# Kernel optimization log

Measured on AMD Instinct MI355X. Metric: run time of the kernel, lower is better.

## Reference

```python
import jax, jax.numpy as jnp
import numpy as np

B, T, V, D = 128, 128, 64, 32
Q, E, PLM = 5, 8, 768
D_STATIC, N_CLASS = 16, 2
ALPHA = 0.5


def _glorot(key, shape):
    lim = (6.0 / (shape[-2] + shape[-1])) ** 0.5
    return jax.random.uniform(key, shape, jnp.float32, -lim, lim)


def setup_inputs() -> dict:
    key = jax.random.key(0)
    ks = jax.random.split(key, 30)
    data = jax.random.normal(ks[0], (B, T, V), jnp.float32)
    mask = (jax.random.uniform(ks[1], (B, T, V)) < 0.3).astype(jnp.float32)
    P = jnp.concatenate([data, mask], axis=-1)  # [b, t, 2v]
    return {
        "P": P,
        "P_static": jax.random.normal(ks[2], (B, D_STATIC), jnp.float32),
        "P_avg_interval": jax.random.uniform(ks[3], (B, T, V)) * 10.0,
        "P_length": jax.random.randint(ks[4], (B, 1), T // 2, T + 1),
        "P_time": jax.random.uniform(ks[5], (B, T)),
        "P_var_plm_rep_tensor": jax.random.normal(ks[6], (V, PLM), jnp.float32),
        # Value_Encoder: Linear(1, D) + ReLU
        "w_val": _glorot(ks[7], (1, D))[0], "b_val": jnp.zeros((D,), jnp.float32),
        # Time_Encoder: periodic Linear(1, D-1), linear Linear(1, 1)
        "w_per": _glorot(ks[8], (1, D - 1))[0], "b_per": jnp.zeros((D - 1,), jnp.float32),
        "w_lin": _glorot(ks[9], (1, 1))[0], "b_lin": jnp.zeros((1,), jnp.float32),
        "emb1": jax.random.normal(ks[10], (V, D), jnp.float32),
        # prior_to_state MLP: PLM -> 2D -> Q
        "Ws1": _glorot(ks[11], (PLM, 2 * D)), "bs1": jnp.zeros((2 * D,), jnp.float32),
        "Ws2": _glorot(ks[12], (2 * D, Q)), "bs2": jnp.zeros((Q,), jnp.float32),
        # prior_to_graph MLP: PLM -> 2D -> E
        "Wg1": _glorot(ks[13], (PLM, 2 * D)), "bg1": jnp.zeros((2 * D,), jnp.float32),
        "Wg2": _glorot(ks[14], (2 * D, E)), "bg2": jnp.zeros((E,), jnp.float32),
        "rarity_W": jax.random.normal(ks[15], (V, V), jnp.float32),
        # hypernet gate params (nodes_num == Q): W [Q, 2D+1, D], b [Q, D]
        "Wu": _glorot(ks[16], (Q, 2 * D + 1, D)), "bu": _glorot(ks[17], (Q, D)),
        "Wr": _glorot(ks[18], (Q, 2 * D + 1, D)), "br": _glorot(ks[19], (Q, D)),
        "Wcand": _glorot(ks[20], (Q, 2 * D + 1, D)), "bcand": _glorot(ks[21], (Q, D)),
        # static embedding + classifier
        "W_se": _glorot(ks[22], (D_STATIC, V)), "b_se": jnp.zeros((V,), jnp.float32),
        "Wc1": _glorot(ks[23], (2 * V, 200)), "bc1": jnp.zeros((200,), jnp.float32),
        "Wc2": _glorot(ks[24], (200, N_CLASS)), "bc2": jnp.zeros((N_CLASS,), jnp.float32),
    }


def _forward(P, P_static, P_avg_interval, P_length, P_time, P_var_plm_rep_tensor,
             w_val, b_val, w_per, b_per, w_lin, b_lin, emb1,
             Ws1, bs1, Ws2, bs2, Wg1, bg1, Wg2, bg2, rarity_W,
             Wu, bu, Wr, br, Wcand, bcand, W_se, b_se, Wc1, bc1, Wc2, bc2):
    b, t, v2 = P.shape
    v = v2 // 2
    d = emb1.shape[1]
    data, mask = P[:, :, :v], P[:, :, v:]            # [b,t,v] each
    mk = mask[..., None]
    # embeddings: value + absolute time + node embedding, all masked
    value_emb = jax.nn.relu(data[..., None] * w_val + b_val) * mk          # [b,t,v,d]
    tt = P_time[:, :, None, None]                                          # [b,t,1,1]
    time_emb = jnp.concatenate([tt * w_lin + b_lin,
                                jnp.sin(tt * w_per + b_per)], -1) * mk     # [b,t,v,d]
    obs_emb = (value_emb + time_emb + emb1[None, None]) * mk               # [b,t,v,d]

    # PLM-prior hypernet vectors (identical across batch -> computed once, broadcast)
    var_vector = jax.nn.relu(P_var_plm_rep_tensor @ Ws1 + bs1) @ Ws2 + bs2  # [v,Q]
    gvec = jax.nn.relu(P_var_plm_rep_tensor @ Wg1 + bg1) @ Wg2 + bg2        # [v,E]
    gvec = gvec / jnp.maximum(jnp.linalg.norm(gvec, axis=-1, keepdims=True), 1e-12)
    adj = jax.nn.softmax(gvec @ gvec.T, axis=-1)                            # [v,v]

    var_total_obs = mask.sum(axis=1)                                        # [b,v]
    eye = jnp.eye(v, dtype=P.dtype)
    lengths = P_length[:, 0].astype(jnp.int32)                              # [b]

    def gate(inp, W, bb):
        # hypernet-generated per-node GRU gate: einsum('nd,dio->nio') + bmm, fused
        return (jnp.einsum('bvi,vq,qio->bvo', inp, var_vector, W)
                + jnp.einsum('vq,qo->vo', var_vector, bb))

    def step(carry, xs):
        h, out = carry
        cur_obs, m, cur_avg, s = xs
        rarity = ALPHA * jnp.tanh(cur_avg / (var_total_obs + 1.0))          # [b,v]
        rsm = -rarity_W * jnp.abs(rarity[:, :, None] - rarity[:, None, :])  # [b,v,v]
        amask = m[:, :, None] * m[:, None, :]   # rows of unobserved zeroed, observed cols = 1
        cur_adj = adj * (1.0 + rsm) * amask * (1.0 - eye) + eye             # [b,v,v]
        x = jnp.concatenate([cur_obs, rarity[..., None]], -1)               # [b,v,d+1]
        comb = jnp.einsum('bij,bjk->bik', cur_adj, jnp.concatenate([x, h], -1))
        r = jax.nn.sigmoid(gate(comb, Wr, br))
        u = jax.nn.sigmoid(gate(comb, Wu, bu))
        h_r = r * h  # original mutates h[nodes_ind] = r*h[nodes_ind] before candidate
        cand = jnp.tanh(gate(jnp.concatenate([x, h_r], -1), Wcand, bcand))
        h_new = (1.0 - u) * h_r + u * cand
        h = jnp.where((m > 0.5)[..., None], h_new, h)  # scatter only observed nodes
        out = jnp.where((s == lengths - 1)[:, None, None], h, out)
        return (h, out), None

    xs = (jnp.moveaxis(obs_emb, 1, 0), jnp.moveaxis(mask, 1, 0),
          jnp.moveaxis(P_avg_interval, 1, 0), jnp.arange(t, dtype=jnp.int32))
    h0 = jnp.zeros((b, v, d), P.dtype)
    (_, output), _ = jax.lax.scan(step, (h0, jnp.zeros_like(h0)), xs)

    static_emb = P_static @ W_se + b_se                                     # [b,v]
    feat = jnp.concatenate([output.sum(-1), static_emb], -1)                # [b,2v]
    return jax.nn.relu(feat @ Wc1 + bc1) @ Wc2 + bc2                        # [b,n_class]


def reference(P, P_static, P_avg_interval, P_length, P_time, P_var_plm_rep_tensor,
              w_val, b_val, w_per, b_per, w_lin, b_lin, emb1,
              Ws1, bs1, Ws2, bs2, Wg1, bg1, Wg2, bg2, rarity_W,
              Wu, bu, Wr, br, Wcand, bcand, W_se, b_se, Wc1, bc1, Wc2, bc2):
    return _forward(P, P_static, P_avg_interval, P_length, P_time, P_var_plm_rep_tensor,
                    w_val, b_val, w_per, b_per, w_lin, b_lin, emb1,
                    Ws1, bs1, Ws2, bs2, Wg1, bg1, Wg2, bg2, rarity_W,
                    Wu, bu, Wr, br, Wcand, bcand, W_se, b_se, Wc1, bc1, Wc2, bc2)
```

## Files before the change

kernel.cpp:

```cpp
#include <hip/hip_runtime.h>
#include <hip/hip_bf16.h>
#include <math.h>

#define BB 128
#define TT 128
#define VV 64
#define DD 32
#define NQ 5

typedef short bf16x8 __attribute__((ext_vector_type(8)));
typedef float f32x4 __attribute__((ext_vector_type(4)));

#define MFMA(a,b,c) __builtin_amdgcn_mfma_f32_16x16x32_bf16(a,b,c,0,0,0)

__device__ __forceinline__ float sigm(float x){ return 1.0f/(1.0f+__expf(-x)); }
__device__ __forceinline__ float tanhfast(float x){ return 2.0f/(1.0f+__expf(-2.0f*x)) - 1.0f; }
__device__ __forceinline__ unsigned short f2bf(float x){
  unsigned u = __float_as_uint(x);
  u += 0x7FFFu + ((u>>16)&1u);
  return (unsigned short)(u>>16);
}
__device__ __forceinline__ float bf2f(unsigned short h){
  return __uint_as_float(((unsigned)h)<<16);
}

union bfu { bf16x8 v; unsigned u[4]; unsigned short s[8]; };

__device__ __forceinline__ void split8(const float* x, bfu& H, bfu& L){
  #pragma unroll
  for (int i = 0; i < 4; ++i){
    const float a = x[2*i], c = x[2*i+1];
    const __hip_bfloat162 hp = __float22bfloat162_rn(make_float2(a, c));
    unsigned hu; __builtin_memcpy(&hu, &hp, 4);
    H.u[i] = hu;
    const float ah = __uint_as_float(hu << 16);
    const float ch = __uint_as_float(hu & 0xFFFF0000u);
    const __hip_bfloat162 lp = __float22bfloat162_rn(make_float2(a - ah, c - ch));
    unsigned lu; __builtin_memcpy(&lu, &lp, 4);
    L.u[i] = lu;
  }
}

__device__ __forceinline__ void split4(const float* x, unsigned* H, unsigned* L){
  #pragma unroll
  for (int i = 0; i < 2; ++i){
    const float a = x[2*i], c = x[2*i+1];
    const __hip_bfloat162 hp = __float22bfloat162_rn(make_float2(a, c));
    unsigned hu; __builtin_memcpy(&hu, &hp, 4);
    H[i] = hu;
    const float ah = __uint_as_float(hu << 16);
    const float ch = __uint_as_float(hu & 0xFFFF0000u);
    const __hip_bfloat162 lp = __float22bfloat162_rn(make_float2(a - ah, c - ch));
    unsigned lu; __builtin_memcpy(&lu, &lp, 4);
    L[i] = lu;
  }
}


__global__ __launch_bounds__(64)
void k_mlp(const float* __restrict__ Pplm,
           const float* __restrict__ Ws1, const float* __restrict__ bs1,
           const float* __restrict__ Ws2, const float* __restrict__ bs2,
           const float* __restrict__ Wg1, const float* __restrict__ bg1,
           const float* __restrict__ Wg2, const float* __restrict__ bg2,
           float* __restrict__ vv_ws, float* __restrict__ gn_ws)
{
  __shared__ float sH[64], sG[64], sgv[8];
  const int v = blockIdx.x, j = threadIdx.x;
  float a = bs1[j], g = bg1[j];
  for (int k = 0; k < 768; ++k){
    const float p = Pplm[v*768 + k];
    a = fmaf(p, Ws1[k*64 + j], a);
    g = fmaf(p, Wg1[k*64 + j], g);
  }
  sH[j] = fmaxf(a, 0.f);
  sG[j] = fmaxf(g, 0.f);
  __syncthreads();
  if (j < 5){
    float acc = bs2[j];
    for (int k = 0; k < 64; ++k) acc = fmaf(sH[k], Ws2[k*5 + j], acc);
    vv_ws[v*5 + j] = acc;
  }
  if (j < 8){
    float acc = bg2[j];
    for (int k = 0; k < 64; ++k) acc = fmaf(sG[k], Wg2[k*8 + j], acc);
    sgv[j] = acc;
  }
  __syncthreads();
  if (j == 0){
    float n = 0.f;
    for (int e = 0; e < 8; ++e) n += sgv[e]*sgv[e];
    n = fmaxf(sqrtf(n), 1e-12f);
    for (int e = 0; e < 8; ++e) gn_ws[v*8 + e] = sgv[e]/n;
  }
}

__global__ __launch_bounds__(64)
void k_adj(const float* __restrict__ gn_ws, float* __restrict__ adj_ws)
{
  const int v = blockIdx.x, j = threadIdx.x;
  float sc = 0.f;
  #pragma unroll
  for (int e = 0; e < 8; ++e) sc += gn_ws[v*8+e]*gn_ws[j*8+e];
  float mx = sc;
  for (int off = 32; off > 0; off >>= 1) mx = fmaxf(mx, __shfl_xor(mx, off));
  const float ex = __expf(sc - mx);
  float sm = ex;
  for (int off = 32; off > 0; off >>= 1) sm += __shfl_xor(sm, off);
  adj_ws[v*64 + j] = ex / sm;
}

__global__ __launch_bounds__(256)
void k_vto(const float* __restrict__ P, float* __restrict__ vto_ws)
{
  const int idx = blockIdx.x*256 + threadIdx.x;
  if (idx >= BB*VV) return;
  const int b = idx/VV, v = idx%VV;
  float s = 0.f;
  for (int t = 0; t < TT; ++t) s += P[((size_t)(b*TT+t))*128 + 64 + v];
  vto_ws[idx] = s;
}

__global__ __launch_bounds__(256)
void k_bpack(const float* __restrict__ Wr, const float* __restrict__ br,
             const float* __restrict__ Wu, const float* __restrict__ bu,
             const float* __restrict__ Wc, const float* __restrict__ bc,
             unsigned short* __restrict__ Bru, unsigned short* __restrict__ Bcn,
             float* __restrict__ sideRU, float* __restrict__ sideC)
{
  const int idx = blockIdx.x*256 + threadIdx.x;
  if (idx < 20480){
    const int f = idx >> 9, rem = idx & 511, l = rem >> 3, j = rem & 7;
    const int p = f & 1, kt = (f>>1)&1, e = f>>2;
    const int kp = kt*32 + (l>>4)*8 + j;
    const int k = (kp < 32) ? kp : kp + 1;
    const int o = p*16 + (l&15);
    const int q = (e < 5) ? e : e - 5;
    const float* W = (e < 5) ? Wr : Wu;
    Bru[idx] = f2bf(W[(q*65 + k)*32 + o]);
  } else if (idx < 30720){
    const int i2 = idx - 20480;
    const int f = i2 >> 9, rem = i2 & 511, l = rem >> 3, j = rem & 7;
    const int p = f & 1, kt = (f>>1)&1, e = f>>2;
    const int kp = kt*32 + (l>>4)*8 + j;
    const int k = (kp < 32) ? kp : kp + 1;
    const int o = p*16 + (l&15);
    Bcn[i2] = f2bf(Wc[(e*65 + k)*32 + o]);
  } else if (idx < 31360){
    const int i3 = idx - 30720;
    const int e = i3 >> 6, rem = i3 & 63, o = rem >> 1, s = rem & 1;
    const int q = (e < 5) ? e : e - 5;
    float v;
    if (s == 0) v = (e < 5) ? Wr[(q*65 + 32)*32 + o] : Wu[(q*65 + 32)*32 + o];
    else        v = (e < 5) ? br[q*32 + o] : bu[q*32 + o];
    sideRU[i3] = v;
  } else if (idx < 31680){
    const int i4 = idx - 31360;
    const int e = i4 >> 6, rem = i4 & 63, o = rem >> 1, s = rem & 1;
    sideC[i4] = s ? bc[e*32 + o] : Wc[(e*65 + 32)*32 + o];
  }
}


__global__ __launch_bounds__(512, 1)
void tedgn_main(const float* __restrict__ P, const float* __restrict__ Pstatic,
                const float* __restrict__ Pavg, const int* __restrict__ Plen,
                const float* __restrict__ Ptime,
                const float* __restrict__ w_val, const float* __restrict__ b_val,
                const float* __restrict__ w_per, const float* __restrict__ b_per,
                const float* __restrict__ w_lin, const float* __restrict__ b_lin,
                const float* __restrict__ emb1, const float* __restrict__ rarW,
                const float* __restrict__ Wse, const float* __restrict__ bse,
                const float* __restrict__ Wc1, const float* __restrict__ bc1,
                const float* __restrict__ Wc2, const float* __restrict__ bc2,
                const float* __restrict__ vv_ws, const float* __restrict__ adjb_ws,
                const float* __restrict__ vto_ws,
                const unsigned short* __restrict__ Bru_ws,
                const unsigned short* __restrict__ Bc_ws,
                const float* __restrict__ sideRU_ws, const float* __restrict__ sideC_ws,
                float* __restrict__ out)
{
  __shared__ __align__(16) unsigned short B0T[2][2][64][72];
  __shared__ __align__(16) unsigned short s_Wru[20480];
  __shared__ __align__(16) unsigned short s_Wc[10240];
  __shared__ __align__(16) float A1f[4][16][68];
  __shared__ __align__(16) float hrF[4][16][36];
  __shared__ __align__(16) float s_rar[2][64];
  __shared__ __align__(16) float s_m[2][64];
  __shared__ float s_sru[640], s_scd[320];
  __shared__ float s_outf[64][33];
  __shared__ float s_feat[128], s_hid[200];

  const int tid  = threadIdx.x;
  const int lane = tid & 63;
  const int wid  = tid >> 6;
  const int mq   = wid >> 1;
  const int ph   = wid & 1;
  const int l15  = lane & 15;
  const int l16g = lane >> 4;
  const int kgo  = l16g * 8;
  const int R    = mq * 16;
  const int v_own = R + l15;
  const int oo   = ph*16 + l15;
  const int b    = blockIdx.x;
  const int len  = Plen[b];

  for (int i = tid; i < 640; i += 512) s_sru[i] = sideRU_ws[i];
  for (int i = tid; i < 320; i += 512) s_scd[i] = sideC_ws[i];
  {
    const uint4* src1 = (const uint4*)Bru_ws;
    uint4* dst1 = (uint4*)s_Wru;
    for (int i = tid; i < 2560; i += 512) dst1[i] = src1[i];
    const uint4* src2 = (const uint4*)Bc_ws;
    uint4* dst2 = (uint4*)s_Wc;
    for (int i = tid; i < 1280; i += 512) dst2[i] = src2[i];
  }

  float adjb_r[2][8], rarW_r[2][8];
  #pragma unroll
  for (int kt = 0; kt < 2; ++kt)
    #pragma unroll
    for (int j = 0; j < 8; ++j){
      adjb_r[kt][j] = adjb_ws[v_own*64 + kt*32 + kgo + j];
      rarW_r[kt][j] = rarW   [v_own*64 + kt*32 + kgo + j];
    }
  float embr[8], wvr[8], bvr[8], wpr[8], bpr[8];
  #pragma unroll
  for (int j = 0; j < 8; ++j){
    const int d = kgo + j;
    embr[j] = emb1[v_own*DD + d];
    wvr[j]  = w_val[d];
    bvr[j]  = b_val[d];
    wpr[j]  = (d == 0) ? w_lin[0] : w_per[d-1];
    bpr[j]  = (d == 0) ? b_lin[0] : b_per[d-1];
  }
  float vvr[4][NQ];
  #pragma unroll
  for (int j = 0; j < 4; ++j)
    #pragma unroll
    for (int q = 0; q < NQ; ++q)
      vvr[j][q] = vv_ws[(R + l16g*4 + j)*NQ + q];
  const float vto_own = vto_ws[b*VV + v_own];

  float h[4]    = {0.f,0.f,0.f,0.f};
  float outr[4] = {0.f,0.f,0.f,0.f};
  bfu xfH, xfL;
  float rar_own, m_own;

  {
    const float pd = P[(size_t)(b*TT)*128 + v_own];
    const float pm = P[(size_t)(b*TT)*128 + 64 + v_own];
    const float pa = Pavg[(size_t)(b*TT)*VV + v_own];
    const float pt = Ptime[b*TT];
    const float rar_n = 0.5f * tanhfast(pa / (vto_own + 1.f));
    float xv[8];
    #pragma unroll
    for (int j = 0; j < 8; ++j){
      const int d = kgo + j;
      const float tearg = fmaf(pt, wpr[j], bpr[j]);
      const float te = (d == 0) ? tearg : __sinf(tearg);
      const float ve = fmaxf(fmaf(pd, wvr[j], bvr[j]), 0.f);
      xv[j] = (ve + te + embr[j]) * pm;
    }
    split8(xv, xfH, xfL);
    if (ph == 0){
      #pragma unroll
      for (int j = 0; j < 8; ++j){
        B0T[0][0][kgo + j][v_own] = xfH.s[j];
        B0T[0][1][kgo + j][v_own] = xfL.s[j];
      }
      *(uint2*)&B0T[0][0][32 + l15][R + l16g*4] = make_uint2(0u, 0u);
      *(uint2*)&B0T[0][1][32 + l15][R + l16g*4] = make_uint2(0u, 0u);
      if (l16g == 0){
        s_rar[0][v_own] = rar_n;
        s_m[0][v_own]   = pm;
      }
    } else {
      *(uint2*)&B0T[0][0][48 + l15][R + l16g*4] = make_uint2(0u, 0u);
      *(uint2*)&B0T[0][1][48 + l15][R + l16g*4] = make_uint2(0u, 0u);
    }
    rar_own = rar_n;
    m_own   = pm;
  }
  __syncthreads();

  #pragma clang loop unroll(disable)
  for (int t = 0; t < TT; ++t){
    const int cur = t & 1, nxt = cur ^ 1;

    float pd = 0.f, pm = 0.f, pa = 0.f, pt = 0.f;
    const bool more = (t + 1 < TT);
    if (more){
      pd = P[(size_t)(b*TT + t + 1)*128 + v_own];
      pm = P[(size_t)(b*TT + t + 1)*128 + 64 + v_own];
      pa = Pavg[(size_t)(b*TT + t + 1)*VV + v_own];
      pt = Ptime[b*TT + t + 1];
    }

    {
      bfu aAh[2], aAl[2];
      float crar = 0.f;
      #pragma unroll
      for (int kt = 0; kt < 2; ++kt){
        const float4 r0 = *(const float4*)&s_rar[cur][kt*32 + kgo];
        const float4 r1 = *(const float4*)&s_rar[cur][kt*32 + kgo + 4];
        const float4 m0 = *(const float4*)&s_m[cur][kt*32 + kgo];
        const float4 m1 = *(const float4*)&s_m[cur][kt*32 + kgo + 4];
        const float rj[8] = {r0.x,r0.y,r0.z,r0.w,r1.x,r1.y,r1.z,r1.w};
        const float mj[8] = {m0.x,m0.y,m0.z,m0.w,m1.x,m1.y,m1.z,m1.w};
        float av[8];
        #pragma unroll
        for (int j = 0; j < 8; ++j){
          const int k = kt*32 + kgo + j;
          const float e1 = fmaf(-rarW_r[kt][j], fabsf(rar_own - rj[j]), 1.0f);
          const float a  = adjb_r[kt][j] * e1 * (m_own * mj[j]);
          av[j] = (k == v_own) ? 1.0f : a;
          crar = fmaf(av[j], rj[j], crar);
        }
        split8(av, aAh[kt], aAl[kt]);
      }
      crar += __shfl_xor(crar, 16);
      crar += __shfl_xor(crar, 32);
      if (ph == 0 && l16g == 0) A1f[mq][l15][64] = crar;

      #pragma unroll
      for (int ni = 0; ni < 2; ++ni){
        const int n = 2*ph + ni;
        f32x4 acc = {0.f,0.f,0.f,0.f};
        #pragma unroll
        for (int kt = 0; kt < 2; ++kt){
          const bf16x8 bh = *(const bf16x8*)&B0T[cur][0][n*16 + l15][kt*32 + kgo];
          const bf16x8 bl = *(const bf16x8*)&B0T[cur][1][n*16 + l15][kt*32 + kgo];
          acc = MFMA(aAh[kt].v, bh, acc);
          acc = MFMA(aAl[kt].v, bh, acc);
          acc = MFMA(aAh[kt].v, bl, acc);
        }
        const int col = n*16 + l15;
        #pragma unroll
        for (int j = 0; j < 4; ++j) A1f[mq][l16g*4 + j][col] = acc[j];
      }
    }
    __syncthreads();

    float hr[4], uu[4];
    {
      bfu aH[2], aL[2];
      #pragma unroll
      for (int kt = 0; kt < 2; ++kt){
        float xv[8];
        *(float4*)&xv[0] = *(const float4*)&A1f[mq][l15][kt*32 + kgo];
        *(float4*)&xv[4] = *(const float4*)&A1f[mq][l15][kt*32 + kgo + 4];
        split8(xv, aH[kt], aL[kt]);
      }
      float a64f[4];
      #pragma unroll
      for (int j = 0; j < 4; ++j) a64f[j] = A1f[mq][l16g*4 + j][64];

      f32x4 ag[10];
      #pragma unroll
      for (int e = 0; e < 10; ++e){
        const float2 wb = *(const float2*)&s_sru[e*64 + oo*2];
        #pragma unroll
        for (int j = 0; j < 4; ++j) ag[e][j] = fmaf(a64f[j], wb.x, wb.y);
      }
      #pragma unroll
      for (int e = 0; e < 10; ++e){
        const bf16x8 w0 = *(const bf16x8*)&s_Wru[(((e*2+0)*2+ph)*64 + lane)*8];
        const bf16x8 w1 = *(const bf16x8*)&s_Wru[(((e*2+1)*2+ph)*64 + lane)*8];
        ag[e] = MFMA(aH[0].v, w0, ag[e]);
        ag[e] = MFMA(aL[0].v, w0, ag[e]);
        ag[e] = MFMA(aH[1].v, w1, ag[e]);
        ag[e] = MFMA(aL[1].v, w1, ag[e]);
      }
      #pragma unroll
      for (int j = 0; j < 4; ++j){
        const float pr = vvr[j][0]*ag[0][j] + vvr[j][1]*ag[1][j]
                       + vvr[j][2]*ag[2][j] + vvr[j][3]*ag[3][j]
                       + vvr[j][4]*ag[4][j];
        hr[j] = sigm(pr) * h[j];
        hrF[mq][l16g*4 + j][oo] = hr[j];
      }
      #pragma unroll
      for (int j = 0; j < 4; ++j){
        const float pu = vvr[j][0]*ag[5][j] + vvr[j][1]*ag[6][j]
                       + vvr[j][2]*ag[7][j] + vvr[j][3]*ag[8][j]
                       + vvr[j][4]*ag[9][j];
        uu[j] = sigm(pu);
      }
    }
    __syncthreads();

    {
      bfu hH, hL;
      {
        float hv[8];
        *(float4*)&hv[0] = *(const float4*)&hrF[mq][l15][kgo];
        *(float4*)&hv[4] = *(const float4*)&hrF[mq][l15][kgo + 4];
        split8(hv, hH, hL);
      }
      float rar_cj[4], m_cj[4];
      #pragma unroll
      for (int j = 0; j < 4; ++j){
        rar_cj[j] = s_rar[cur][R + l16g*4 + j];
        m_cj[j]   = s_m[cur][R + l16g*4 + j];
      }
      f32x4 ag[5];
      #pragma unroll
      for (int e = 0; e < 5; ++e){
        const float2 wb = *(const float2*)&s_scd[e*64 + oo*2];
        #pragma unroll
        for (int j = 0; j < 4; ++j) ag[e][j] = fmaf(rar_cj[j], wb.x, wb.y);
      }
      #pragma unroll
      for (int e = 0; e < 5; ++e){
        const bf16x8 w0 = *(const bf16x8*)&s_Wc[(((e*2+0)*2+ph)*64 + lane)*8];
        const bf16x8 w1 = *(const bf16x8*)&s_Wc[(((e*2+1)*2+ph)*64 + lane)*8];
        ag[e] = MFMA(xfH.v, w0, ag[e]);
        ag[e] = MFMA(xfL.v, w0, ag[e]);
        ag[e] = MFMA(hH.v,  w1, ag[e]);
        ag[e] = MFMA(hL.v,  w1, ag[e]);
      }
      const bool snap = (t == len - 1);
      #pragma unroll
      for (int j = 0; j < 4; ++j){
        const float pc = vvr[j][0]*ag[0][j] + vvr[j][1]*ag[1][j]
                       + vvr[j][2]*ag[2][j] + vvr[j][3]*ag[3][j]
                       + vvr[j][4]*ag[4][j];
        const float cd = tanhfast(pc);
        const float hn = fmaf(uu[j], cd - hr[j], hr[j]);
        const float hf = (m_cj[j] > 0.5f) ? hn : h[j];
        h[j] = hf;
        if (snap) outr[j] = hf;
      }
      {
        unsigned H2[2], L2[2];
        split4(h, H2, L2);
        *(uint2*)&B0T[nxt][0][32 + oo][R + l16g*4] = make_uint2(H2[0], H2[1]);
        *(uint2*)&B0T[nxt][1][32 + oo][R + l16g*4] = make_uint2(L2[0], L2[1]);
      }
      if (more){
        const float rar_n = 0.5f * tanhfast(pa / (vto_own + 1.f));
        float xv[8];
        #pragma unroll
        for (int j = 0; j < 8; ++j){
          const int d = kgo + j;
          const float tearg = fmaf(pt, wpr[j], bpr[j]);
          const float te = (d == 0) ? tearg : __sinf(tearg);
          const float ve = fmaxf(fmaf(pd, wvr[j], bvr[j]), 0.f);
          xv[j] = (ve + te + embr[j]) * pm;
        }
        split8(xv, xfH, xfL);
        if (ph == 0){
          #pragma unroll
          for (int j = 0; j < 8; ++j){
            B0T[nxt][0][kgo + j][v_own] = xfH.s[j];
            B0T[nxt][1][kgo + j][v_own] = xfL.s[j];
          }
          if (l16g == 0){
            s_rar[nxt][v_own] = rar_n;
            s_m[nxt][v_own]   = pm;
          }
        }
        rar_own = rar_n;
        m_own   = pm;
      }
    }
    __syncthreads();
  }

  #pragma unroll
  for (int j = 0; j < 4; ++j)
    s_outf[R + l16g*4 + j][oo] = outr[j];
  __syncthreads();
  if (tid < VV){
    float s = 0.f;
    #pragma unroll
    for (int d = 0; d < DD; ++d) s += s_outf[tid][d];
    s_feat[tid] = s;
  } else if (tid < 2*VV){
    const int v = tid - VV;
    float se = bse[v];
    #pragma unroll
    for (int k = 0; k < 16; ++k) se = fmaf(Pstatic[b*16 + k], Wse[k*VV + v], se);
    s_feat[VV + v] = se;
  }
  __syncthreads();
  if (tid < 200){
    float a = bc1[tid];
    for (int k = 0; k < 128; ++k) a = fmaf(s_feat[k], Wc1[k*200 + tid], a);
    s_hid[tid] = fmaxf(a, 0.f);
  }
  __syncthreads();
  if (tid < 2){
    float a = bc2[tid];
    for (int k = 0; k < 200; ++k) a = fmaf(s_hid[k], Wc2[k*2 + tid], a);
    out[b*2 + tid] = a;
  }
}


extern "C" void kernel_launch(void* const* d_in, const int* in_sizes, int n_in,
                              void* d_out, int out_size, void* d_ws, size_t ws_size,
                              hipStream_t stream) {
  (void)in_sizes; (void)n_in; (void)out_size; (void)ws_size;
  const float* P       = (const float*)d_in[0];
  const float* Pstatic = (const float*)d_in[1];
  const float* Pavg    = (const float*)d_in[2];
  const int*   Plen    = (const int*)  d_in[3];
  const float* Ptime   = (const float*)d_in[4];
  const float* Pplm    = (const float*)d_in[5];
  const float* w_val   = (const float*)d_in[6];
  const float* b_val   = (const float*)d_in[7];
  const float* w_per   = (const float*)d_in[8];
  const float* b_per   = (const float*)d_in[9];
  const float* w_lin   = (const float*)d_in[10];
  const float* b_lin   = (const float*)d_in[11];
  const float* emb1    = (const float*)d_in[12];
  const float* Ws1     = (const float*)d_in[13];
  const float* bs1     = (const float*)d_in[14];
  const float* Ws2     = (const float*)d_in[15];
  const float* bs2     = (const float*)d_in[16];
  const float* Wg1     = (const float*)d_in[17];
  const float* bg1     = (const float*)d_in[18];
  const float* Wg2     = (const float*)d_in[19];
  const float* bg2     = (const float*)d_in[20];
  const float* rarW    = (const float*)d_in[21];
  const float* Wu      = (const float*)d_in[22];
  const float* bu      = (const float*)d_in[23];
  const float* Wr      = (const float*)d_in[24];
  const float* br      = (const float*)d_in[25];
  const float* Wcand   = (const float*)d_in[26];
  const float* bcand   = (const float*)d_in[27];
  const float* Wse     = (const float*)d_in[28];
  const float* bse     = (const float*)d_in[29];
  const float* Wc1     = (const float*)d_in[30];
  const float* bc1     = (const float*)d_in[31];
  const float* Wc2     = (const float*)d_in[32];
  const float* bc2     = (const float*)d_in[33];

  float* ws = (float*)d_ws;
  float*          vv_ws   = ws;
  float*          gn_ws   = ws + 320;
  float*          adjb_ws = ws + 832;
  float*          vto_ws  = ws + 4928;
  unsigned short* Bru_ws  = (unsigned short*)(ws + 13120);
  unsigned short* Bc_ws   = (unsigned short*)(ws + 23360);
  float*          sideRU_ws = ws + 28480;
  float*          sideC_ws  = ws + 29120;

  k_mlp  <<<64, 64, 0, stream>>>(Pplm, Ws1, bs1, Ws2, bs2, Wg1, bg1, Wg2, bg2, vv_ws, gn_ws);
  k_adj  <<<64, 64, 0, stream>>>(gn_ws, adjb_ws);
  k_vto  <<<(BB*VV + 255)/256, 256, 0, stream>>>(P, vto_ws);
  k_bpack<<<124, 256, 0, stream>>>(Wr, br, Wu, bu, Wcand, bcand, Bru_ws, Bc_ws, sideRU_ws, sideC_ws);

  tedgn_main<<<BB, 512, 0, stream>>>(P, Pstatic, Pavg, Plen, Ptime,
                                     w_val, b_val, w_per, b_per, w_lin, b_lin,
                                     emb1, rarW, Wse, bse, Wc1, bc1, Wc2, bc2,
                                     vv_ws, adjb_ws, vto_ws,
                                     Bru_ws, Bc_ws, sideRU_ws, sideC_ws,
                                     (float*)d_out);
}
```

Before: 586.2 us.

## Add producer wavefronts to precompute next-step adjacency fragments during recurrence

Grows the block from 8 to 12 wavefronts. The four new producer waves compute the next timestep's adjacency matrix, its bf16 hi/lo split fragments, the rarity-weighted row sums and the input embeddings, and write them into double-buffered shared memory. The worker waves now read these precomputed A fragments instead of rebuilding the adjacency every step, which removes that work from the serial recurrence's critical path. In exchange the block uses more shared memory and threads, producers must keep pace within the existing barrier phases, and the classifier scratch buffers are aliased onto the fragment buffer.

New measurement: 741.5 us. +26.5%, slower.

```diff
diff --git a/kernel.cpp b/kernel.cpp
--- a/kernel.cpp
+++ b/kernel.cpp
@@ -38,21 +38,6 @@
     const __hip_bfloat162 lp = __float22bfloat162_rn(make_float2(a - ah, c - ch));
     unsigned lu; __builtin_memcpy(&lu, &lp, 4);
     L.u[i] = lu;
-  }
-}
-
-__device__ __forceinline__ void split4(const float* x, unsigned* H, unsigned* L){
-  #pragma unroll
-  for (int i = 0; i < 2; ++i){
-    const float a = x[2*i], c = x[2*i+1];
-    const __hip_bfloat162 hp = __float22bfloat162_rn(make_float2(a, c));
-    unsigned hu; __builtin_memcpy(&hu, &hp, 4);
-    H[i] = hu;
-    const float ah = __uint_as_float(hu << 16);
-    const float ch = __uint_as_float(hu & 0xFFFF0000u);
-    const __hip_bfloat162 lp = __float22bfloat162_rn(make_float2(a - ah, c - ch));
-    unsigned lu; __builtin_memcpy(&lu, &lp, 4);
-    L[i] = lu;
   }
 }
 
@@ -162,7 +147,7 @@
 }
 
 
-__global__ __launch_bounds__(512, 1)
+__global__ __launch_bounds__(768, 1)
 void tedgn_main(const float* __restrict__ P, const float* __restrict__ Pstatic,
                 const float* __restrict__ Pavg, const int* __restrict__ Plen,
                 const float* __restrict__ Ptime,
@@ -183,18 +168,19 @@
   __shared__ __align__(16) unsigned short B0T[2][2][64][72];
   __shared__ __align__(16) unsigned short s_Wru[20480];
   __shared__ __align__(16) unsigned short s_Wc[10240];
+  __shared__ __align__(16) unsigned short sFragA[2][4][2][2][64][8];
   __shared__ __align__(16) float A1f[4][16][68];
   __shared__ __align__(16) float hrF[4][16][36];
   __shared__ __align__(16) float s_rar[2][64];
   __shared__ __align__(16) float s_m[2][64];
+  __shared__ float s_crar[2][64];
   __shared__ float s_sru[640], s_scd[320];
-  __shared__ float s_outf[64][33];
-  __shared__ float s_feat[128], s_hid[200];
 
   const int tid  = threadIdx.x;
   const int lane = tid & 63;
   const int wid  = tid >> 6;
-  const int mq   = wid >> 1;
+  const bool isWork = (wid < 8);
+  const int mq   = isWork ? (wid >> 1) : (wid - 8);
   const int ph   = wid & 1;
   const int l15  = lane & 15;
   const int l16g = lane >> 4;
@@ -205,25 +191,17 @@
   const int b    = blockIdx.x;
   const int len  = Plen[b];
 
-  for (int i = tid; i < 640; i += 512) s_sru[i] = sideRU_ws[i];
-  for (int i = tid; i < 320; i += 512) s_scd[i] = sideC_ws[i];
+  for (int i = tid; i < 640; i += 768) s_sru[i] = sideRU_ws[i];
+  for (int i = tid; i < 320; i += 768) s_scd[i] = sideC_ws[i];
   {
     const uint4* src1 = (const uint4*)Bru_ws;
     uint4* dst1 = (uint4*)s_Wru;
-    for (int i = tid; i < 2560; i += 512) dst1[i] = src1[i];
+    for (int i = tid; i < 2560; i += 768) dst1[i] = src1[i];
     const uint4* src2 = (const uint4*)Bc_ws;
     uint4* dst2 = (uint4*)s_Wc;
-    for (int i = tid; i < 1280; i += 512) dst2[i] = src2[i];
-  }
-
-  float adjb_r[2][8], rarW_r[2][8];
-  #pragma unroll
-  for (int kt = 0; kt < 2; ++kt)
-    #pragma unroll
-    for (int j = 0; j < 8; ++j){
-      adjb_r[kt][j] = adjb_ws[v_own*64 + kt*32 + kgo + j];
-      rarW_r[kt][j] = rarW   [v_own*64 + kt*32 + kgo + j];
-    }
+    for (int i = tid; i < 1280; i += 768) dst2[i] = src2[i];
+  }
+
   float embr[8], wvr[8], bvr[8], wpr[8], bpr[8];
   #pragma unroll
   for (int j = 0; j < 8; ++j){
@@ -234,25 +212,36 @@
     wpr[j]  = (d == 0) ? w_lin[0] : w_per[d-1];
     bpr[j]  = (d == 0) ? b_lin[0] : b_per[d-1];
   }
+
+  float adjb_r[2][8], rarW_r[2][8];
+  float vto_own = 0.f;
   float vvr[4][NQ];
-  #pragma unroll
-  for (int j = 0; j < 4; ++j)
-    #pragma unroll
-    for (int q = 0; q < NQ; ++q)
-      vvr[j][q] = vv_ws[(R + l16g*4 + j)*NQ + q];
-  const float vto_own = vto_ws[b*VV + v_own];
+  if (!isWork){
+    #pragma unroll
+    for (int kt = 0; kt < 2; ++kt)
+      #pragma unroll
+      for (int j = 0; j < 8; ++j){
+        adjb_r[kt][j] = adjb_ws[v_own*64 + kt*32 + kgo + j];
+        rarW_r[kt][j] = rarW   [v_own*64 + kt*32 + kgo + j];
+      }
+    vto_own = vto_ws[b*VV + v_own];
+  } else {
+    #pragma unroll
+    for (int j = 0; j < 4; ++j)
+      #pragma unroll
+      for (int q = 0; q < NQ; ++q)
+        vvr[j][q] = vv_ws[(R + l16g*4 + j)*NQ + q];
+  }
 
   float h[4]    = {0.f,0.f,0.f,0.f};
   float outr[4] = {0.f,0.f,0.f,0.f};
-  bfu xfH, xfL;
-  float rar_own, m_own;
-
-  {
+  bfu xfH, xfL, xfnH, xfnL;
+  float pp_pd = 0.f, pp_pm = 0.f, pp_pt = 0.f, pp_rar = 0.f;
+
+  if (isWork){
     const float pd = P[(size_t)(b*TT)*128 + v_own];
     const float pm = P[(size_t)(b*TT)*128 + 64 + v_own];
-    const float pa = Pavg[(size_t)(b*TT)*VV + v_own];
     const float pt = Ptime[b*TT];
-    const float rar_n = 0.5f * tanhfast(pa / (vto_own + 1.f));
     float xv[8];
     #pragma unroll
     for (int j = 0; j < 8; ++j){
@@ -264,86 +253,136 @@
     }
     split8(xv, xfH, xfL);
     if (ph == 0){
-      #pragma unroll
-      for (int j = 0; j < 8; ++j){
-        B0T[0][0][kgo + j][v_own] = xfH.s[j];
-        B0T[0][1][kgo + j][v_own] = xfL.s[j];
-      }
       *(uint2*)&B0T[0][0][32 + l15][R + l16g*4] = make_uint2(0u, 0u);
       *(uint2*)&B0T[0][1][32 + l15][R + l16g*4] = make_uint2(0u, 0u);
-      if (l16g == 0){
-        s_rar[0][v_own] = rar_n;
-        s_m[0][v_own]   = pm;
-      }
     } else {
       *(uint2*)&B0T[0][0][48 + l15][R + l16g*4] = make_uint2(0u, 0u);
       *(uint2*)&B0T[0][1][48 + l15][R + l16g*4] = make_uint2(0u, 0u);
     }
-    rar_own = rar_n;
-    m_own   = pm;
+  } else {
+    pp_pd = P[(size_t)(b*TT)*128 + v_own];
+    pp_pm = P[(size_t)(b*TT)*128 + 64 + v_own];
+    const float pa = Pavg[(size_t)(b*TT)*VV + v_own];
+    pp_pt = Ptime[b*TT];
+    pp_rar = 0.5f * tanhfast(pa / (vto_own + 1.f));
+    if (l16g == 0){
+      s_rar[0][v_own] = pp_rar;
+      s_m[0][v_own]   = pp_pm;
+    }
+  }
+  __syncthreads();
+  if (!isWork){
+    float xv[8];
+    #pragma unroll
+    for (int j = 0; j < 8; ++j){
+      const int d = kgo + j;
+      const float tearg = fmaf(pp_pt, wpr[j], bpr[j]);
+      const float te = (d == 0) ? tearg : __sinf(tearg);
+      const float ve = fmaxf(fmaf(pp_pd, wvr[j], bvr[j]), 0.f);
+      xv[j] = (ve + te + embr[j]) * pp_pm;
+    }
+    bfu xh, xl;
+    split8(xv, xh, xl);
+    #pragma unroll
+    for (int j = 0; j < 8; ++j){
+      B0T[0][0][kgo + j][v_own] = xh.s[j];
+      B0T[0][1][kgo + j][v_own] = xl.s[j];
+    }
+    bfu aAh[2], aAl[2];
+    float crar = 0.f;
+    #pragma unroll
+    for (int kt = 0; kt < 2; ++kt){
+      const float4 r0 = *(const float4*)&s_rar[0][kt*32 + kgo];
+      const float4 r1 = *(const float4*)&s_rar[0][kt*32 + kgo + 4];
+      const float4 m0 = *(const float4*)&s_m[0][kt*32 + kgo];
+      const float4 m1 = *(const float4*)&s_m[0][kt*32 + kgo + 4];
+      const float rj[8] = {r0.x,r0.y,r0.z,r0.w,r1.x,r1.y,r1.z,r1.w};
+      const float mj[8] = {m0.x,m0.y,m0.z,m0.w,m1.x,m1.y,m1.z,m1.w};
+      float av[8];
+      #pragma unroll
+      for (int j = 0; j < 8; ++j){
+        const int k = kt*32 + kgo + j;
+        const float e1 = fmaf(-rarW_r[kt][j], fabsf(pp_rar - rj[j]), 1.0f);
+        const float a  = adjb_r[kt][j] * e1 * (pp_pm * mj[j]);
+        av[j] = (k == v_own) ? 1.0f : a;
+        crar = fmaf(av[j], rj[j], crar);
+      }
+      split8(av, aAh[kt], aAl[kt]);
+    }
+    crar += __shfl_xor(crar, 16);
+    crar += __shfl_xor(crar, 32);
+    if (l16g == 0) s_crar[0][v_own] = crar;
+    #pragma unroll
+    for (int kt = 0; kt < 2; ++kt){
+      *(bf16x8*)&sFragA[0][mq][kt][0][lane][0] = aAh[kt].v;
+      *(bf16x8*)&sFragA[0][mq][kt][1][lane][0] = aAl[kt].v;
+    }
   }
   __syncthreads();
 
   #pragma clang loop unroll(disable)
   for (int t = 0; t < TT; ++t){
     const int cur = t & 1, nxt = cur ^ 1;
-
-    float pd = 0.f, pm = 0.f, pa = 0.f, pt = 0.f;
     const bool more = (t + 1 < TT);
-    if (more){
-      pd = P[(size_t)(b*TT + t + 1)*128 + v_own];
-      pm = P[(size_t)(b*TT + t + 1)*128 + 64 + v_own];
-      pa = Pavg[(size_t)(b*TT + t + 1)*VV + v_own];
-      pt = Ptime[b*TT + t + 1];
-    }
-
-    {
-      bfu aAh[2], aAl[2];
-      float crar = 0.f;
-      #pragma unroll
-      for (int kt = 0; kt < 2; ++kt){
-        const float4 r0 = *(const float4*)&s_rar[cur][kt*32 + kgo];
-        const float4 r1 = *(const float4*)&s_rar[cur][kt*32 + kgo + 4];
-        const float4 m0 = *(const float4*)&s_m[cur][kt*32 + kgo];
-        const float4 m1 = *(const float4*)&s_m[cur][kt*32 + kgo + 4];
-        const float rj[8] = {r0.x,r0.y,r0.z,r0.w,r1.x,r1.y,r1.z,r1.w};
-        const float mj[8] = {m0.x,m0.y,m0.z,m0.w,m1.x,m1.y,m1.z,m1.w};
-        float av[8];
-        #pragma unroll
-        for (int j = 0; j < 8; ++j){
-          const int k = kt*32 + kgo + j;
-          const float e1 = fmaf(-rarW_r[kt][j], fabsf(rar_own - rj[j]), 1.0f);
-          const float a  = adjb_r[kt][j] * e1 * (m_own * mj[j]);
-          av[j] = (k == v_own) ? 1.0f : a;
-          crar = fmaf(av[j], rj[j], crar);
-        }
-        split8(av, aAh[kt], aAl[kt]);
-      }
-      crar += __shfl_xor(crar, 16);
-      crar += __shfl_xor(crar, 32);
-      if (ph == 0 && l16g == 0) A1f[mq][l15][64] = crar;
-
+
+    if (isWork){
+      float pd = 0.f, pm = 0.f, pt = 0.f;
+      if (more){
+        pd = P[(size_t)(b*TT + t + 1)*128 + v_own];
+        pm = P[(size_t)(b*TT + t + 1)*128 + 64 + v_own];
+        pt = Ptime[b*TT + t + 1];
+      }
+      bf16x8 aAh0 = *(const bf16x8*)&sFragA[cur][mq][0][0][lane][0];
+      bf16x8 aAl0 = *(const bf16x8*)&sFragA[cur][mq][0][1][lane][0];
+      bf16x8 aAh1 = *(const bf16x8*)&sFragA[cur][mq][1][0][lane][0];
+      bf16x8 aAl1 = *(const bf16x8*)&sFragA[cur][mq][1][1][lane][0];
       #pragma unroll
       for (int ni = 0; ni < 2; ++ni){
         const int n = 2*ph + ni;
         f32x4 acc = {0.f,0.f,0.f,0.f};
-        #pragma unroll
-        for (int kt = 0; kt < 2; ++kt){
-          const bf16x8 bh = *(const bf16x8*)&B0T[cur][0][n*16 + l15][kt*32 + kgo];
-          const bf16x8 bl = *(const bf16x8*)&B0T[cur][1][n*16 + l15][kt*32 + kgo];
-          acc = MFMA(aAh[kt].v, bh, acc);
-          acc = MFMA(aAl[kt].v, bh, acc);
-          acc = MFMA(aAh[kt].v, bl, acc);
+        {
+          const bf16x8 bh0 = *(const bf16x8*)&B0T[cur][0][n*16 + l15][kgo];
+          const bf16x8 bl0 = *(const bf16x8*)&B0T[cur][1][n*16 + l15][kgo];
+          acc = MFMA(aAh0, bh0, acc);
+          acc = MFMA(aAl0, bh0, acc);
+          acc = MFMA(aAh0, bl0, acc);
+          const bf16x8 bh1 = *(const bf16x8*)&B0T[cur][0][n*16 + l15][32 + kgo];
+          const bf16x8 bl1 = *(const bf16x8*)&B0T[cur][1][n*16 + l15][32 + kgo];
+          acc = MFMA(aAh1, bh1, acc);
+          acc = MFMA(aAl1, bh1, acc);
+          acc = MFMA(aAh1, bl1, acc);
         }
         const int col = n*16 + l15;
         #pragma unroll
         for (int j = 0; j < 4; ++j) A1f[mq][l16g*4 + j][col] = acc[j];
       }
+      if (more){
+        float xv[8];
+        #pragma unroll
+        for (int j = 0; j < 8; ++j){
+          const int d = kgo + j;
+          const float tearg = fmaf(pt, wpr[j], bpr[j]);
+          const float te = (d == 0) ? tearg : __sinf(tearg);
+          const float ve = fmaxf(fmaf(pd, wvr[j], bvr[j]), 0.f);
+          xv[j] = (ve + te + embr[j]) * pm;
+        }
+        split8(xv, xfnH, xfnL);
+      }
+    } else if (more){
+      pp_pd = P[(size_t)(b*TT + t + 1)*128 + v_own];
+      pp_pm = P[(size_t)(b*TT + t + 1)*128 + 64 + v_own];
+      const float pa = Pavg[(size_t)(b*TT + t + 1)*VV + v_own];
+      pp_pt = Ptime[b*TT + t + 1];
+      pp_rar = 0.5f * tanhfast(pa / (vto_own + 1.f));
+      if (l16g == 0){
+        s_rar[nxt][v_own] = pp_rar;
+        s_m[nxt][v_own]   = pp_pm;
+      }
     }
     __syncthreads();
 
     float hr[4], uu[4];
-    {
+    if (isWork){
       bfu aH[2], aL[2];
       #pragma unroll
       for (int kt = 0; kt < 2; ++kt){
@@ -354,7 +393,7 @@
       }
       float a64f[4];
       #pragma unroll
-      for (int j = 0; j < 4; ++j) a64f[j] = A1f[mq][l16g*4 + j][64];
+      for (int j = 0; j < 4; ++j) a64f[j] = s_crar[cur][R + l16g*4 + j];
 
       f32x4 ag[10];
       #pragma unroll
@@ -387,10 +426,56 @@
                        + vvr[j][4]*ag[9][j];
         uu[j] = sigm(pu);
       }
+    } else if (more){
+      float xv[8];
+      #pragma unroll
+      for (int j = 0; j < 8; ++j){
+        const int d = kgo + j;
+        const float tearg = fmaf(pp_pt, wpr[j], bpr[j]);
+        const float te = (d == 0) ? tearg : __sinf(tearg);
+        const float ve = fmaxf(fmaf(pp_pd, wvr[j], bvr[j]), 0.f);
+        xv[j] = (ve + te + embr[j]) * pp_pm;
+      }
+      bfu xh, xl;
+      split8(xv, xh, xl);
+      #pragma unroll
+      for (int j = 0; j < 8; ++j){
+        B0T[nxt][0][kgo + j][v_own] = xh.s[j];
+        B0T[nxt][1][kgo + j][v_own] = xl.s[j];
+      }
+      bfu aAh[2], aAl[2];
+      float crar = 0.f;
+      #pragma unroll
+      for (int kt = 0; kt < 2; ++kt){
+        const float4 r0 = *(const float4*)&s_rar[nxt][kt*32 + kgo];
+        const float4 r1 = *(const float4*)&s_rar[nxt][kt*32 + kgo + 4];
+        const float4 m0 = *(const float4*)&s_m[nxt][kt*32 + kgo];
+        const float4 m1 = *(const float4*)&s_m[nxt][kt*32 + kgo + 4];
+        const float rj[8] = {r0.x,r0.y,r0.z,r0.w,r1.x,r1.y,r1.z,r1.w};
+        const float mj[8] = {m0.x,m0.y,m0.z,m0.w,m1.x,m1.y,m1.z,m1.w};
+        float av[8];
+        #pragma unroll
+        for (int j = 0; j < 8; ++j){
+          const int k = kt*32 + kgo + j;
+          const float e1 = fmaf(-rarW_r[kt][j], fabsf(pp_rar - rj[j]), 1.0f);
+          const float a  = adjb_r[kt][j] * e1 * (pp_pm * mj[j]);
+          av[j] = (k == v_own) ? 1.0f : a;
+          crar = fmaf(av[j], rj[j], crar);
+        }
+        split8(av, aAh[kt], aAl[kt]);
+      }
+      crar += __shfl_xor(crar, 16);
+      crar += __shfl_xor(crar, 32);
+      if (l16g == 0) s_crar[nxt][v_own] = crar;
+      #pragma unroll
+      for (int kt = 0; kt < 2; ++kt){
+        *(bf16x8*)&sFragA[nxt][mq][kt][0][lane][0] = aAh[kt].v;
+        *(bf16x8*)&sFragA[nxt][mq][kt][1][lane][0] = aAl[kt].v;
+      }
     }
     __syncthreads();
 
-    {
+    if (isWork){
       bfu hH, hL;
       {
         float hv[8];
@@ -434,48 +519,39 @@
       }
       {
         unsigned H2[2], L2[2];
-        split4(h, H2, L2);
+        #pragma unroll
+        for (int i = 0; i < 2; ++i){
+          const float a = h[2*i], c = h[2*i+1];
+          const __hip_bfloat162 hp = __float22bfloat162_rn(make_float2(a, c));
+          unsigned hu; __builtin_memcpy(&hu, &hp, 4);
+          H2[i] = hu;
+          const float ah = __uint_as_float(hu << 16);
+          const float ch = __uint_as_float(hu & 0xFFFF0000u);
+          const __hip_bfloat162 lp = __float22bfloat162_rn(make_float2(a - ah, c - ch));
+          unsigned lu; __builtin_memcpy(&lu, &lp, 4);
+          L2[i] = lu;
+        }
         *(uint2*)&B0T[nxt][0][32 + oo][R + l16g*4] = make_uint2(H2[0], H2[1]);
         *(uint2*)&B0T[nxt][1][32 + oo][R + l16g*4] = make_uint2(L2[0], L2[1]);
       }
-      if (more){
-        const float rar_n = 0.5f * tanhfast(pa / (vto_own + 1.f));
-        float xv[8];
-        #pragma unroll
-        for (int j = 0; j < 8; ++j){
-          const int d = kgo + j;
-          const float tearg = fmaf(pt, wpr[j], bpr[j]);
-          const float te = (d == 0) ? tearg : __sinf(tearg);
-          const float ve = fmaxf(fmaf(pd, wvr[j], bvr[j]), 0.f);
-          xv[j] = (ve + te + embr[j]) * pm;
-        }
-        split8(xv, xfH, xfL);
-        if (ph == 0){
-          #pragma unroll
-          for (int j = 0; j < 8; ++j){
-            B0T[nxt][0][kgo + j][v_own] = xfH.s[j];
-            B0T[nxt][1][kgo + j][v_own] = xfL.s[j];
-          }
-          if (l16g == 0){
-            s_rar[nxt][v_own] = rar_n;
-            s_m[nxt][v_own]   = pm;
-          }
-        }
-        rar_own = rar_n;
-        m_own   = pm;
-      }
+      if (more){ xfH = xfnH; xfL = xfnL; }
     }
     __syncthreads();
   }
 
-  #pragma unroll
-  for (int j = 0; j < 4; ++j)
-    s_outf[R + l16g*4 + j][oo] = outr[j];
+  float* s_outf = (float*)sFragA;
+  float* s_feat = s_outf + 64*33;
+  float* s_hid  = s_feat + 128;
+  if (isWork){
+    #pragma unroll
+    for (int j = 0; j < 4; ++j)
+      s_outf[(R + l16g*4 + j)*33 + oo] = outr[j];
+  }
   __syncthreads();
   if (tid < VV){
     float s = 0.f;
     #pragma unroll
-    for (int d = 0; d < DD; ++d) s += s_outf[tid][d];
+    for (int d = 0; d < DD; ++d) s += s_outf[tid*33 + d];
     s_feat[tid] = s;
   } else if (tid < 2*VV){
     const int v = tid - VV;
@@ -553,7 +629,7 @@
   k_vto  <<<(BB*VV + 255)/256, 256, 0, stream>>>(P, vto_ws);
   k_bpack<<<124, 256, 0, stream>>>(Wr, br, Wu, bu, Wcand, bcand, Bru_ws, Bc_ws, sideRU_ws, sideC_ws);
 
-  tedgn_main<<<BB, 512, 0, stream>>>(P, Pstatic, Pavg, Plen, Ptime,
+  tedgn_main<<<BB, 768, 0, stream>>>(P, Pstatic, Pavg, Plen, Ptime,
                                      w_val, b_val, w_per, b_per, w_lin, b_lin,
                                      emb1, rarW, Wse, bse, Wc1, bc1, Wc2, bc2,
                                      vv_ws, adjb_ws, vto_ws,
```
